# Optimization experiments

Measured on AMD Instinct MI355X. Metric: run time of the kernel, lower is better.

The kernel has to match this reference:

```python
import jax, jax.numpy as jnp
import numpy as np

P0, P1 = 64, 4            # partition_size
NH, HD = 32, 16           # num_heads, head_dim
N = P0 * P1               # attn_area = tokens per window
B = 64                    # number of windows
C = 3 * NH * HD           # packed qkv channels


def _rel_index_1d(T):
    # relative_position_index from get_relative_position_index_1d
    idx = np.arange(T)
    return jnp.asarray(idx[:, None] - idx[None, :] + (T - 1))  # (T, T) in [0, 2T-2]


def setup_inputs() -> dict:
    key = jax.random.key(0)
    k1, k2 = jax.random.split(key)
    inp = jax.random.normal(k1, (B, N, C), dtype=jnp.float32)
    table = jax.random.normal(k2, (2 * P0 - 1, NH), dtype=jnp.float32) * 0.02
    return {"input": inp, "rel_bias_table": table}


def reference(input, rel_bias_table):
    Bq, Nq, Cq = input.shape
    hd = Cq // (3 * NH)
    # (B, N, 3, H, D) -> (3, B, H, N, D)
    qkv = input.reshape(Bq, Nq, 3, NH, hd).transpose(2, 0, 3, 1, 4)
    q, k, v = qkv[0], qkv[1], qkv[2]
    q = q * (NH ** -0.5)  # module scales by num_heads**-0.5 (as in source)
    attn = jnp.einsum('bhnd,bhmd->bhnm', q, k)  # (B, H, N, N)
    # type_1 relative positional bias: gather (P0,P0,H), tile over P1 on both axes
    rel_idx = _rel_index_1d(P0)
    bias = rel_bias_table[rel_idx]                       # (P0, P0, H)
    bias = jnp.broadcast_to(bias[:, None, :, None, :], (P0, P1, P0, P1, NH))
    bias = bias.reshape(N, N, NH).transpose(2, 0, 1)     # (H, N, N)
    attn = attn + bias[None]
    attn = jax.nn.softmax(attn, axis=-1)
    out = jnp.einsum('bhnm,bhmd->bhnd', attn, v)         # (B, H, N, D)
    return out.transpose(0, 2, 1, 3).reshape(Bq, Nq, NH * hd)
```

## Files before the change

### kernel.cpp

```cpp
#include <hip/hip_runtime.h>
#include <hip/hip_bf16.h>


typedef short bf16x8 __attribute__((ext_vector_type(8)));
typedef float f32x16 __attribute__((ext_vector_type(16)));

__device__ __forceinline__ unsigned int pk2(float a, float b) {
  __hip_bfloat162 hh = __float22bfloat162_rn(float2{a, b});
  unsigned int u; __builtin_memcpy(&u, &hh, 4); return u;
}

#if __has_builtin(__builtin_amdgcn_permlane32_swap)
typedef int i32x2_t __attribute__((ext_vector_type(2)));
__device__ __forceinline__ void swap_halves(unsigned x, unsigned y, unsigned& ox, unsigned& oy) {
  i32x2_t r = __builtin_amdgcn_permlane32_swap((int)x, (int)y, false, false);
  ox = (unsigned)r.x;
  oy = (unsigned)r.y;
}
#else
__device__ __forceinline__ void swap_halves(unsigned x, unsigned y, unsigned& ox, unsigned& oy) {
  const int hi = (threadIdx.x & 63) >> 5;
  unsigned tx = (unsigned)__shfl_xor((int)x, 32);
  unsigned ty = (unsigned)__shfl_xor((int)y, 32);
  ox = hi ? ty : x;
  oy = hi ? y : tx;
}
#endif

__global__ void mhsa_kernel(const float* __restrict__ inp, const float* __restrict__ table,
                            float* __restrict__ out) {
  const int bid = blockIdx.x;
  const int bh = ((bid & 7) << 8) | (bid >> 3);
  const int b = bh >> 5, h = bh & 31;
  const int t = threadIdx.x;
  const int l = t & 63;
  const int w = t >> 6;
  const int q32 = l & 31;
  const int hi = l >> 5;

  __shared__ __align__(16) short KF[8][64][8];
  __shared__ __align__(16) short VF[16][34][8];
  __shared__ float tbl[128];

  const float* gbase = inp + (size_t)b * (256 * 1536) + h * 16;
  const int row0 = t >> 2, c4 = t & 3;

  const float* p0 = gbase + (size_t)(row0      ) * 1536 + c4 * 4;
  const float* p1 = gbase + (size_t)(row0 +  64) * 1536 + c4 * 4;
  const float* p2 = gbase + (size_t)(row0 + 128) * 1536 + c4 * 4;
  const float* p3 = gbase + (size_t)(row0 + 192) * 1536 + c4 * 4;
  float4 ka = *(const float4*)(p0 + 512);
  float4 va = *(const float4*)(p0 + 1024);
  float4 kb_ = *(const float4*)(p1 + 512);
  float4 vb_ = *(const float4*)(p1 + 1024);
  float4 kc = *(const float4*)(p2 + 512);
  float4 vc = *(const float4*)(p2 + 1024);
  float4 kd = *(const float4*)(p3 + 512);
  float4 vd = *(const float4*)(p3 + 1024);
  const float* qp0 = gbase + (size_t)(w * 32 + q32) * 1536 + hi * 8;
  const float* qp1 = qp0 + 4 * 32 * 1536;
  float4 qa0 = *(const float4*)qp0;
  float4 qb0 = *(const float4*)(qp0 + 4);
  float4 qa1 = *(const float4*)qp1;
  float4 qb1 = *(const float4*)(qp1 + 4);

  if (t < 127) tbl[t] = table[t * 32 + h] * 1.4426950408889634f;
  {
    const int kb = t >> 4, hv = (t >> 3) & 1, j = t & 7;
    VF[kb][hv * 17 + 16][j] = (short)0x3F80;
  }

  auto stage = [&](int row, const float4& kv, const float4& vv) {
    short* kdst = &KF[0][0][0] + (row >> 5) * 512 + ((c4 >> 1) * 32 + (row & 31)) * 8 + (c4 & 1) * 4;
    *(int2*)kdst = make_int2(pk2(kv.x, kv.y), pk2(kv.z, kv.w));
    unsigned v01 = pk2(vv.x, vv.y), v23 = pk2(vv.z, vv.w);
    short* vdst = &VF[0][0][0] + (row >> 4) * 272 + (((row >> 3) & 1) * 17 + c4 * 4) * 8 + (row & 7);
    vdst[0]  = (short)(v01 & 0xffff);
    vdst[8]  = (short)(v01 >> 16);
    vdst[16] = (short)(v23 & 0xffff);
    vdst[24] = (short)(v23 >> 16);
  };
  stage(row0, ka, va);
  stage(row0 + 64, kb_, vb_);
  stage(row0 + 128, kc, vc);
  stage(row0 + 192, kd, vd);

  bf16x8 q8A, q8B;
  { unsigned qw[4] = { pk2(qa0.x, qa0.y), pk2(qa0.z, qa0.w),
                       pk2(qb0.x, qb0.y), pk2(qb0.z, qb0.w) };
    __builtin_memcpy(&q8A, qw, 16); }
  { unsigned qw[4] = { pk2(qa1.x, qa1.y), pk2(qa1.z, qa1.w),
                       pk2(qb1.x, qb1.y), pk2(qb1.z, qb1.w) };
    __builtin_memcpy(&q8B, qw, 16); }

  __syncthreads();

  const float scale2 = 0.17677669529663687f * 1.4426950408889634f;
  const f32x16 z16 = {0.f};
  const short* kfb = &KF[0][0][0] + l * 8;
  const int vslot = hi * 17 + (q32 > 16 ? 16 : q32);
  const short* vfb = &VF[0][0][0] + vslot * 8;

  auto body = [&](int kt, const f32x16& s, f32x16& o, int bb) {
    unsigned wd[8];
    #pragma unroll
    for (int m = 0; m < 4; ++m) {
      const float bias = tbl[bb - kt * 8 - 2 * m];
      float e0 = __builtin_amdgcn_exp2f(fmaf(s[4 * m + 0], scale2, bias));
      float e1 = __builtin_amdgcn_exp2f(fmaf(s[4 * m + 1], scale2, bias));
      float e2 = __builtin_amdgcn_exp2f(fmaf(s[4 * m + 2], scale2, bias));
      float e3 = __builtin_amdgcn_exp2f(fmaf(s[4 * m + 3], scale2, bias));
      wd[2 * m]     = pk2(e0, e1);
      wd[2 * m + 1] = pk2(e2, e3);
    }
    unsigned f0, f1, f2, f3;
    bf16x8 pf0, pf1;
    swap_halves(wd[0], wd[2], f0, f2);
    swap_halves(wd[1], wd[3], f1, f3);
    { unsigned a4[4] = { f0, f1, f2, f3 }; __builtin_memcpy(&pf0, a4, 16); }
    swap_halves(wd[4], wd[6], f0, f2);
    swap_halves(wd[5], wd[7], f1, f3);
    { unsigned a4[4] = { f0, f1, f2, f3 }; __builtin_memcpy(&pf1, a4, 16); }
    bf16x8 v0 = *(const bf16x8*)(vfb + (kt * 2 + 0) * 272);
    bf16x8 v1 = *(const bf16x8*)(vfb + (kt * 2 + 1) * 272);
    o = __builtin_amdgcn_mfma_f32_32x32x16_bf16(v0, pf0, o, 0, 0, 0);
    o = __builtin_amdgcn_mfma_f32_32x32x16_bf16(v1, pf1, o, 0, 0, 0);
  };

  auto attend = [&](const bf16x8& q8, int qbase) -> f32x16 {
    f32x16 o = z16;
    const int bb = (qbase >> 2) + (q32 >> 2) + 63 - hi;
    bf16x8 kf0 = *(const bf16x8*)kfb;
    f32x16 s = __builtin_amdgcn_mfma_f32_32x32x16_bf16(kf0, q8, z16, 0, 0, 0);
    #pragma unroll
    for (int kt = 0; kt < 7; ++kt) {
      bf16x8 kfn = *(const bf16x8*)(kfb + (kt + 1) * 512);
      f32x16 s_next = __builtin_amdgcn_mfma_f32_32x32x16_bf16(kfn, q8, z16, 0, 0, 0);
      body(kt, s, o, bb);
      s = s_next;
    }
    body(7, s, o, bb);
    return o;
  };

  auto store = [&](const f32x16& o, int qbase) {
    const float inv = 1.0f / __shfl(o[8], q32);
    float* op = out + (size_t)(b * 256 + qbase + q32) * 512 + h * 16 + hi * 4;
    float4 r0 = { o[0] * inv, o[1] * inv, o[2] * inv, o[3] * inv };
    float4 r1 = { o[4] * inv, o[5] * inv, o[6] * inv, o[7] * inv };
    *(float4*)op = r0;
    *(float4*)(op + 8) = r1;
  };

  f32x16 oA = attend(q8A, w * 32);
  store(oA, w * 32);
  f32x16 oB = attend(q8B, (w + 4) * 32);
  store(oB, (w + 4) * 32);
}

extern "C" void kernel_launch(void* const* d_in, const int* in_sizes, int n_in,
                              void* d_out, int out_size, void* d_ws, size_t ws_size,
                              hipStream_t stream) {
  (void)in_sizes; (void)n_in; (void)out_size; (void)d_ws; (void)ws_size;
  const float* inp = (const float*)d_in[0];
  const float* tbl = (const float*)d_in[1];
  float* out = (float*)d_out;
  hipLaunchKernelGGL(mhsa_kernel, dim3(2048), dim3(256), 0, stream, inp, tbl, out);
}
```

Before: 38.80 us.

## Double block size so each wave handles one query tile

Launches 512 threads per block instead of 256, so there are eight waves per block. Each wave now processes a single 32-query tile rather than two in sequence, and each thread stages two K/V rows instead of four. This shortens each wave's serial chain of MFMA and exp work and raises the number of waves available to hide latency. The cost is more threads sharing the fixed per-block setup and possibly more register pressure per CU.

```diff
diff --git a/kernel.cpp b/kernel.cpp
--- a/kernel.cpp
+++ b/kernel.cpp
@@ -45,27 +45,18 @@
   const float* gbase = inp + (size_t)b * (256 * 1536) + h * 16;
   const int row0 = t >> 2, c4 = t & 3;
 
-  const float* p0 = gbase + (size_t)(row0      ) * 1536 + c4 * 4;
-  const float* p1 = gbase + (size_t)(row0 +  64) * 1536 + c4 * 4;
-  const float* p2 = gbase + (size_t)(row0 + 128) * 1536 + c4 * 4;
-  const float* p3 = gbase + (size_t)(row0 + 192) * 1536 + c4 * 4;
+  const float* p0 = gbase + (size_t)row0 * 1536 + c4 * 4;
+  const float* p1 = gbase + (size_t)(row0 + 128) * 1536 + c4 * 4;
   float4 ka = *(const float4*)(p0 + 512);
   float4 va = *(const float4*)(p0 + 1024);
   float4 kb_ = *(const float4*)(p1 + 512);
   float4 vb_ = *(const float4*)(p1 + 1024);
-  float4 kc = *(const float4*)(p2 + 512);
-  float4 vc = *(const float4*)(p2 + 1024);
-  float4 kd = *(const float4*)(p3 + 512);
-  float4 vd = *(const float4*)(p3 + 1024);
-  const float* qp0 = gbase + (size_t)(w * 32 + q32) * 1536 + hi * 8;
-  const float* qp1 = qp0 + 4 * 32 * 1536;
-  float4 qa0 = *(const float4*)qp0;
-  float4 qb0 = *(const float4*)(qp0 + 4);
-  float4 qa1 = *(const float4*)qp1;
-  float4 qb1 = *(const float4*)(qp1 + 4);
+  const float* qp = gbase + (size_t)(w * 32 + q32) * 1536 + hi * 8;
+  float4 qa = *(const float4*)qp;
+  float4 qb = *(const float4*)(qp + 4);
 
   if (t < 127) tbl[t] = table[t * 32 + h] * 1.4426950408889634f;
-  {
+  if (t < 256) {
     const int kb = t >> 4, hv = (t >> 3) & 1, j = t & 7;
     VF[kb][hv * 17 + 16][j] = (short)0x3F80;
   }
@@ -81,17 +72,12 @@
     vdst[24] = (short)(v23 >> 16);
   };
   stage(row0, ka, va);
-  stage(row0 + 64, kb_, vb_);
-  stage(row0 + 128, kc, vc);
-  stage(row0 + 192, kd, vd);
+  stage(row0 + 128, kb_, vb_);
 
-  bf16x8 q8A, q8B;
-  { unsigned qw[4] = { pk2(qa0.x, qa0.y), pk2(qa0.z, qa0.w),
-                       pk2(qb0.x, qb0.y), pk2(qb0.z, qb0.w) };
-    __builtin_memcpy(&q8A, qw, 16); }
-  { unsigned qw[4] = { pk2(qa1.x, qa1.y), pk2(qa1.z, qa1.w),
-                       pk2(qb1.x, qb1.y), pk2(qb1.z, qb1.w) };
-    __builtin_memcpy(&q8B, qw, 16); }
+  bf16x8 q8;
+  { unsigned qw[4] = { pk2(qa.x, qa.y), pk2(qa.z, qa.w),
+                       pk2(qb.x, qb.y), pk2(qb.z, qb.w) };
+    __builtin_memcpy(&q8, qw, 16); }
 
   __syncthreads();
 
@@ -101,7 +87,10 @@
   const int vslot = hi * 17 + (q32 > 16 ? 16 : q32);
   const short* vfb = &VF[0][0][0] + vslot * 8;
 
-  auto body = [&](int kt, const f32x16& s, f32x16& o, int bb) {
+  const int qbase = w * 32;
+  const int bb = (qbase >> 2) + (q32 >> 2) + 63 - hi;
+
+  auto body = [&](int kt, const f32x16& s, f32x16& o) {
     unsigned wd[8];
     #pragma unroll
     for (int m = 0; m < 4; ++m) {
@@ -127,35 +116,26 @@
     o = __builtin_amdgcn_mfma_f32_32x32x16_bf16(v1, pf1, o, 0, 0, 0);
   };
 
-  auto attend = [&](const bf16x8& q8, int qbase) -> f32x16 {
-    f32x16 o = z16;
-    const int bb = (qbase >> 2) + (q32 >> 2) + 63 - hi;
+  f32x16 o = z16;
+  {
     bf16x8 kf0 = *(const bf16x8*)kfb;
     f32x16 s = __builtin_amdgcn_mfma_f32_32x32x16_bf16(kf0, q8, z16, 0, 0, 0);
     #pragma unroll
     for (int kt = 0; kt < 7; ++kt) {
       bf16x8 kfn = *(const bf16x8*)(kfb + (kt + 1) * 512);
       f32x16 s_next = __builtin_amdgcn_mfma_f32_32x32x16_bf16(kfn, q8, z16, 0, 0, 0);
-      body(kt, s, o, bb);
+      body(kt, s, o);
       s = s_next;
     }
-    body(7, s, o, bb);
-    return o;
-  };
+    body(7, s, o);
+  }
 
-  auto store = [&](const f32x16& o, int qbase) {
-    const float inv = 1.0f / __shfl(o[8], q32);
-    float* op = out + (size_t)(b * 256 + qbase + q32) * 512 + h * 16 + hi * 4;
-    float4 r0 = { o[0] * inv, o[1] * inv, o[2] * inv, o[3] * inv };
-    float4 r1 = { o[4] * inv, o[5] * inv, o[6] * inv, o[7] * inv };
-    *(float4*)op = r0;
-    *(float4*)(op + 8) = r1;
-  };
-
-  f32x16 oA = attend(q8A, w * 32);
-  store(oA, w * 32);
-  f32x16 oB = attend(q8B, (w + 4) * 32);
-  store(oB, (w + 4) * 32);
+  const float inv = 1.0f / __shfl(o[8], q32);
+  float* op = out + (size_t)(b * 256 + qbase + q32) * 512 + h * 16 + hi * 4;
+  float4 r0 = { o[0] * inv, o[1] * inv, o[2] * inv, o[3] * inv };
+  float4 r1 = { o[4] * inv, o[5] * inv, o[6] * inv, o[7] * inv };
+  *(float4*)op = r0;
+  *(float4*)(op + 8) = r1;
 }
 
 extern "C" void kernel_launch(void* const* d_in, const int* in_sizes, int n_in,
@@ -165,5 +145,5 @@
   const float* inp = (const float*)d_in[0];
   const float* tbl = (const float*)d_in[1];
   float* out = (float*)d_out;
-  hipLaunchKernelGGL(mhsa_kernel, dim3(2048), dim3(256), 0, stream, inp, tbl, out);
+  hipLaunchKernelGGL(mhsa_kernel, dim3(2048), dim3(512), 0, stream, inp, tbl, out);
 }
```

Measured after the change: 36.03 us. 1.08x faster.
